# Optimization experiments

Hardware: AMD Instinct MI355X
Metric: run time of the kernel (lower is better)

Reference implementation:

```python
import jax, jax.numpy as jnp
import numpy as np

B, S, DMODEL, HEADS = 2, 2048, 1024, 16
DK = DMODEL // HEADS
DV = DMODEL // HEADS


def setup_inputs() -> dict:
    key = jax.random.key(0)
    kx, kq, kk, kv = jax.random.split(key, 4)
    x = jax.random.normal(kx, (B, S, DMODEL), dtype=jnp.float32)
    # stacked per-head projection weights, shape [H, dmodel, dk/dv]
    # (equivalent to nn.Linear(dmodel, dk, bias=False) per head)
    scale = 1.0 / np.sqrt(DMODEL)
    Wq = jax.random.uniform(kq, (HEADS, DMODEL, DK), jnp.float32, -scale, scale)
    Wk = jax.random.uniform(kk, (HEADS, DMODEL, DK), jnp.float32, -scale, scale)
    Wv = jax.random.uniform(kv, (HEADS, DMODEL, DV), jnp.float32, -scale, scale)
    return {"x": x, "Wq": Wq, "Wk": Wk, "Wv": Wv}


def reference(x, Wq, Wk, Wv):
    # per-head projections, batched across heads: [B,H,S,dk]
    q = jnp.einsum("bsd,hdk->bhsk", x, Wq)
    k = jnp.einsum("bsd,hdk->bhsk", x, Wk)
    v = jnp.einsum("bsd,hdv->bhsv", x, Wv)
    # NOTE: original module applies NO 1/sqrt(dk) scaling — keep faithful
    scores = jnp.einsum("bhqk,bhsk->bhqs", q, k)  # [B,H,S,S]
    attn = jax.nn.softmax(scores, axis=-1)
    out = jnp.einsum("bhqs,bhsv->bhqv", attn, v)  # [B,H,S,dv]
    # concat heads along last dim in head order
    Bsz, H, Sq, Dv = out.shape
    return jnp.transpose(out, (0, 2, 1, 3)).reshape(Bsz, Sq, H * Dv)
```

## Files before the change

### kernel.cpp

```cpp
#include <hip/hip_runtime.h>

#define B_ 2
#define S_ 2048
#define D_ 1024
#define H_ 16
#define DK_ 64
#define M_ (B_ * S_)
#define N_ (3 * D_)

typedef __bf16 bf16x8 __attribute__((ext_vector_type(8)));
typedef short s8vec __attribute__((ext_vector_type(8)));
typedef float f4vec __attribute__((ext_vector_type(4)));

static __device__ __forceinline__ ushort f2b(float f) {
  union { float f; unsigned u; } v; v.f = f;
  unsigned u = v.u;
  u += 0x7FFFu + ((u >> 16) & 1u);
  return (ushort)(u >> 16);
}

static __device__ __forceinline__ unsigned pk2(float a, float b) {
#if __has_builtin(__builtin_amdgcn_cvt_pk_bf16_f32)
  typedef __bf16 b2 __attribute__((ext_vector_type(2)));
  b2 r = __builtin_amdgcn_cvt_pk_bf16_f32(a, b);
  return __builtin_bit_cast(unsigned, r);
#else
  return (unsigned)f2b(a) | ((unsigned)f2b(b) << 16);
#endif
}

static __device__ __forceinline__ float fexp2(float x) {
#if __has_builtin(__builtin_amdgcn_exp2f)
  return __builtin_amdgcn_exp2f(x);
#else
  return exp2f(x);
#endif
}

static __device__ __forceinline__ f4vec mfma16(s8vec a, s8vec b, f4vec c) {
  return __builtin_amdgcn_mfma_f32_16x16x32_bf16(
      __builtin_bit_cast(bf16x8, a), __builtin_bit_cast(bf16x8, b), c, 0, 0, 0);
}

static __device__ __forceinline__ void gl_lds16(const ushort* g, ushort* l) {
  __builtin_amdgcn_global_load_lds(
      (const __attribute__((address_space(1))) unsigned*)g,
      (__attribute__((address_space(3))) unsigned*)l, 16, 0, 0);
}

static __device__ __forceinline__ void wg_barrier_lds() {
  asm volatile("" ::: "memory");
  __builtin_amdgcn_s_waitcnt(0xC07F);
  __builtin_amdgcn_s_barrier();
  asm volatile("" ::: "memory");
}

__global__ __launch_bounds__(256) void cvt_all(const float* __restrict__ x,
                                               const float* __restrict__ Wq,
                                               const float* __restrict__ Wk,
                                               const float* __restrict__ Wv,
                                               ushort* __restrict__ xb,
                                               ushort* __restrict__ wbt) {
  const int t = threadIdx.x;
  if (blockIdx.x < 4096) {
    int i = blockIdx.x * 256 + t;
    float4 v = ((const float4*)x)[i];
    ushort4 o;
    o.x = f2b(v.x); o.y = f2b(v.y); o.z = f2b(v.z); o.w = f2b(v.w);
    ((ushort4*)xb)[i] = o;
  } else {
    __shared__ ushort T[64 * 72];
    int bid = blockIdx.x - 4096;
    int w = bid >> 8, rem = bid & 255;
    int h = rem >> 4, d0 = (rem & 15) * 64;
    const float* W = (w == 0) ? Wq : (w == 1) ? Wk : Wv;
    const float* src = W + (size_t)h * 65536 + (size_t)d0 * 64;
#pragma unroll
    for (int j = 0; j < 4; ++j) {
      int idx = j * 256 + t;
      int dr = idx >> 4, kc = (idx & 15) * 4;
      float4 v = *(const float4*)(src + dr * 64 + kc);
      T[(kc + 0) * 72 + dr] = f2b(v.x);
      T[(kc + 1) * 72 + dr] = f2b(v.y);
      T[(kc + 2) * 72 + dr] = f2b(v.z);
      T[(kc + 3) * 72 + dr] = f2b(v.w);
    }
    __syncthreads();
    const int kk = t >> 2, dcg = (t & 3) * 16;
    ushort* dst = wbt + ((size_t)w * 1024 + h * 64 + kk) * 1024 + d0 + dcg;
    *(s8vec*)dst       = *(const s8vec*)&T[kk * 72 + dcg];
    *(s8vec*)(dst + 8) = *(const s8vec*)&T[kk * 72 + dcg + 8];
  }
}

__global__ __launch_bounds__(256) void proj_gemm(const ushort* __restrict__ xb,
                                                 const ushort* __restrict__ wbt,
                                                 ushort* __restrict__ qkv) {
  __shared__ __attribute__((aligned(16))) ushort As[128 * 64];
  __shared__ __attribute__((aligned(16))) ushort Bs[128 * 64];
  const int tid = threadIdx.x, wid = tid >> 6, lane = tid & 63;
  const int quad = lane >> 4, l15 = lane & 15;
  const int wm = wid & 1, wn = wid >> 1;
  const int m0 = blockIdx.x * 128, n0 = blockIdx.y * 128;

  f4vec acc[4][4];
#pragma unroll
  for (int mb = 0; mb < 4; mb++)
#pragma unroll
    for (int nb = 0; nb < 4; nb++)
#pragma unroll
      for (int i = 0; i < 4; i++) acc[mb][nb][i] = 0.f;

  const int sr = tid >> 3, sg = tid & 7;
  const int lg = sg ^ (sr & 7);
  const ushort* Ab = xb + (size_t)m0 * D_;
  const ushort* Bb = wbt + (size_t)n0 * D_;

  for (int k0 = 0; k0 < D_; k0 += 64) {
    __syncthreads();
#pragma unroll
    for (int j = 0; j < 4; ++j) {
      int r = j * 32 + sr;
      gl_lds16(Ab + (size_t)r * D_ + k0 + lg * 8, &As[j * 2048 + wid * 512]);
      gl_lds16(Bb + (size_t)r * D_ + k0 + lg * 8, &Bs[j * 2048 + wid * 512]);
    }
    __syncthreads();

#pragma unroll
    for (int kb = 0; kb < 2; ++kb) {
      s8vec af[4], bf[4];
#pragma unroll
      for (int mb = 0; mb < 4; ++mb) {
        int m = wm * 64 + mb * 16 + l15;
        int gpos = (kb * 4 + quad) ^ (m & 7);
        af[mb] = *(const s8vec*)&As[m * 64 + gpos * 8];
      }
#pragma unroll
      for (int nb = 0; nb < 4; ++nb) {
        int n = wn * 64 + nb * 16 + l15;
        int gpos = (kb * 4 + quad) ^ (n & 7);
        bf[nb] = *(const s8vec*)&Bs[n * 64 + gpos * 8];
      }
#pragma unroll
      for (int mb = 0; mb < 4; ++mb)
#pragma unroll
        for (int nb = 0; nb < 4; ++nb)
          acc[mb][nb] = mfma16(af[mb], bf[nb], acc[mb][nb]);
    }
  }

  const size_t per = (size_t)B_ * H_ * S_ * DK_;
  const int w = n0 >> 10;
  if (w == 2) {
    ushort* vt = qkv + 2 * per;
#pragma unroll
    for (int mb = 0; mb < 4; ++mb)
#pragma unroll
      for (int nb = 0; nb < 4; ++nb)
#pragma unroll
        for (int i = 0; i < 4; ++i) {
          int m = m0 + wm * 64 + mb * 16 + quad * 4 + i;
          int b = m >> 11, s = m & 2047;
          int n1 = (n0 & 1023) + wn * 64 + nb * 16 + l15;
          vt[((size_t)b * 1024 + n1) * S_ + s] = f2b(acc[mb][nb][i]);
        }
  } else {
    const float qs = (w == 0) ? 1.44269504f : 1.0f;
#pragma unroll
    for (int mb = 0; mb < 4; ++mb)
#pragma unroll
      for (int nb = 0; nb < 4; ++nb)
#pragma unroll
        for (int i = 0; i < 4; ++i) {
          int m = m0 + wm * 64 + mb * 16 + quad * 4 + i;
          int b = m >> 11, s = m & 2047;
          int n1 = (n0 & 1023) + wn * 64 + nb * 16 + l15;
          qkv[(size_t)w * per + (((size_t)b * H_ + (n1 >> 6)) * S_ + s) * 64 + (n1 & 63)] =
              f2b(acc[mb][nb][i] * qs);
        }
  }
}

__global__ __launch_bounds__(256) void attn(const ushort* __restrict__ qg,
                                            const ushort* __restrict__ kg,
                                            const ushort* __restrict__ vtg,
                                            float* __restrict__ out) {
  __shared__ __attribute__((aligned(16))) ushort Ks[64 * 64];
  __shared__ __attribute__((aligned(16))) ushort Vt[64 * 64];
  __shared__ __attribute__((aligned(16))) ushort Ps[4][32 * 128];
  const int qt = blockIdx.x, bh = blockIdx.y;
  const int b = bh >> 4, h = bh & 15;
  const int tid = threadIdx.x, wid = tid >> 6, lane = tid & 63;
  const int quad = lane >> 4, l15 = lane & 15, l7 = l15 & 7;

  const ushort* qbase = qg + ((size_t)bh * S_ + qt * 128 + wid * 32) * DK_;
  s8vec aq[2][2];
#pragma unroll
  for (int mb = 0; mb < 2; mb++) {
    aq[mb][0] = *(const s8vec*)(qbase + (size_t)(mb * 16 + l15) * DK_ + quad * 8);
    aq[mb][1] = *(const s8vec*)(qbase + (size_t)(mb * 16 + l15) * DK_ + 32 + quad * 8);
  }

  f4vec o[2][4];
  float lsum[2];
#pragma unroll
  for (int mb = 0; mb < 2; mb++) {
    lsum[mb] = 0.f;
#pragma unroll
    for (int nb = 0; nb < 4; nb++)
#pragma unroll
      for (int i = 0; i < 4; i++) o[mb][nb][i] = 0.f;
  }

  const int r = tid >> 3, gs = tid & 7;
  const int gk = gs ^ (r & 7);
  const ushort* kb_ = kg + (size_t)bh * S_ * DK_;
  const ushort* vb_ = vtg + (size_t)bh * 64 * S_;

  s8vec kpre[2], vpre[2];
  kpre[0] = *(const s8vec*)(kb_ + (size_t)r * DK_ + gk * 8);
  kpre[1] = *(const s8vec*)(kb_ + (size_t)(r + 32) * DK_ + gk * 8);
  vpre[0] = *(const s8vec*)(vb_ + (size_t)r * S_ + gk * 8);
  vpre[1] = *(const s8vec*)(vb_ + (size_t)(r + 32) * S_ + gk * 8);

  for (int kt = 0; kt < S_ / 64; ++kt) {
    wg_barrier_lds();
    *(s8vec*)&Ks[r * 64 + gs * 8]        = kpre[0];
    *(s8vec*)&Ks[(r + 32) * 64 + gs * 8] = kpre[1];
    *(s8vec*)&Vt[r * 64 + gs * 8]        = vpre[0];
    *(s8vec*)&Vt[(r + 32) * 64 + gs * 8] = vpre[1];
    if (kt + 1 < S_ / 64) {
      const ushort* kn = kb_ + (size_t)((kt + 1) * 64 + r) * DK_ + gk * 8;
      kpre[0] = *(const s8vec*)(kn);
      kpre[1] = *(const s8vec*)(kn + (size_t)32 * DK_);
      const ushort* vn = vb_ + (size_t)r * S_ + (kt + 1) * 64 + gk * 8;
      vpre[0] = *(const s8vec*)(vn);
      vpre[1] = *(const s8vec*)(vn + (size_t)32 * S_);
    }
    wg_barrier_lds();

    f4vec sct[2][4];
#pragma unroll
    for (int nb = 0; nb < 4; nb++) {
      const int row = nb * 16 + l15;
      s8vec ak0 = *(const s8vec*)&Ks[row * 64 + ((0 + quad) ^ l7) * 8];
      s8vec ak1 = *(const s8vec*)&Ks[row * 64 + ((4 + quad) ^ l7) * 8];
#pragma unroll
      for (int mb = 0; mb < 2; mb++) {
        f4vec z;
#pragma unroll
        for (int i = 0; i < 4; i++) z[i] = 0.f;
        z = mfma16(ak0, aq[mb][0], z);
        sct[mb][nb] = mfma16(ak1, aq[mb][1], z);
      }
    }

#pragma unroll
    for (int mb = 0; mb < 2; mb++) {
      const int q = mb * 16 + l15;
#pragma unroll
      for (int nb = 0; nb < 4; nb++) {
#pragma unroll
        for (int i = 0; i < 4; i++) {
          float p = fexp2(sct[mb][nb][i]);
          sct[mb][nb][i] = p;
          lsum[mb] += p;
        }
        unsigned p01 = pk2(sct[mb][nb][0], sct[mb][nb][1]);
        unsigned p23 = pk2(sct[mb][nb][2], sct[mb][nb][3]);
        const int c = (nb * 2 + (quad >> 1)) ^ l7;
        *(uint2*)&Ps[wid][q * 128 + c * 8 + (quad & 1) * 4] = make_uint2(p01, p23);
      }
    }

#pragma unroll
    for (int kc = 0; kc < 2; kc++) {
      s8vec ap[2];
#pragma unroll
      for (int mb = 0; mb < 2; mb++)
        ap[mb] = *(const s8vec*)&Ps[wid][(mb * 16 + l15) * 128 + (((kc * 4 + quad)) ^ l7) * 8];
#pragma unroll
      for (int nb = 0; nb < 4; nb++) {
        s8vec av = *(const s8vec*)&Vt[(nb * 16 + l15) * 64 + ((kc * 4 + quad) ^ l7) * 8];
        o[0][nb] = mfma16(av, ap[0], o[0][nb]);
        o[1][nb] = mfma16(av, ap[1], o[1][nb]);
      }
    }
  }

#pragma unroll
  for (int mb = 0; mb < 2; mb++) {
    lsum[mb] += __shfl_xor(lsum[mb], 16, 64);
    lsum[mb] += __shfl_xor(lsum[mb], 32, 64);
  }

#pragma unroll
  for (int mb = 0; mb < 2; mb++) {
    const float inv = 1.0f / lsum[mb];
    float* ob = out + ((size_t)b * S_ + qt * 128 + wid * 32 + mb * 16 + l15) * D_ + h * DK_;
#pragma unroll
    for (int nb = 0; nb < 4; nb++) {
      float4 v;
      v.x = o[mb][nb][0] * inv;
      v.y = o[mb][nb][1] * inv;
      v.z = o[mb][nb][2] * inv;
      v.w = o[mb][nb][3] * inv;
      *(float4*)(ob + nb * 16 + quad * 4) = v;
    }
  }
}

extern "C" void kernel_launch(void* const* d_in, const int* in_sizes, int n_in,
                              void* d_out, int out_size, void* d_ws, size_t ws_size,
                              hipStream_t stream) {
  const float* x  = (const float*)d_in[0];
  const float* Wq = (const float*)d_in[1];
  const float* Wk = (const float*)d_in[2];
  const float* Wv = (const float*)d_in[3];
  float* out = (float*)d_out;

  ushort* xb  = (ushort*)d_ws;
  ushort* wbt = xb + (size_t)B_ * S_ * D_;
  ushort* qkv = wbt + (size_t)3 * D_ * D_;
  const size_t per = (size_t)B_ * H_ * S_ * DK_;

  cvt_all<<<4096 + 768, 256, 0, stream>>>(x, Wq, Wk, Wv, xb, wbt);
  proj_gemm<<<dim3(M_ / 128, N_ / 128), 256, 0, stream>>>(xb, wbt, qkv);
  attn<<<dim3(S_ / 128, B_ * H_), 256, 0, stream>>>(qkv, qkv + per, qkv + 2 * per, out);
}
```

Measured before the change: 177.5 us.

## Split attention key range across two blocks and reduce partials

Adds a split-K dimension to the attention grid so each block handles half the key sequence, which doubles the block count from 512 to 1024 to fill the GPU better. Each half writes unnormalized fp32 partial outputs and row sums, and a new reduce kernel combines them. The row sum is now computed on the MFMA units by appending rows of ones to the V tile (an extra nb block) instead of scalar adds. The cost is extra global traffic for the fp32 partials and one more kernel launch. The workspace is reordered so the partials reuse the xb/wbt buffers.

```diff
diff --git a/kernel.cpp b/kernel.cpp
--- a/kernel.cpp
+++ b/kernel.cpp
@@ -184,14 +184,22 @@
 __global__ __launch_bounds__(256) void attn(const ushort* __restrict__ qg,
                                             const ushort* __restrict__ kg,
                                             const ushort* __restrict__ vtg,
-                                            float* __restrict__ out) {
+                                            float* __restrict__ opart,
+                                            float* __restrict__ lpart) {
   __shared__ __attribute__((aligned(16))) ushort Ks[64 * 64];
-  __shared__ __attribute__((aligned(16))) ushort Vt[64 * 64];
-  __shared__ __attribute__((aligned(16))) ushort Ps[4][32 * 128];
-  const int qt = blockIdx.x, bh = blockIdx.y;
+  __shared__ __attribute__((aligned(16))) ushort Vt[80 * 64];
+  __shared__ __attribute__((aligned(16))) ushort Ps[4][32 * 64];
+  const int qt = blockIdx.x, bh = blockIdx.y, ks = blockIdx.z;
   const int b = bh >> 4, h = bh & 15;
   const int tid = threadIdx.x, wid = tid >> 6, lane = tid & 63;
   const int quad = lane >> 4, l15 = lane & 15, l7 = l15 & 7;
+  const int kt0 = ks * (S_ / 128);
+
+  if (tid < 128) {
+    ushort* p = &Vt[(64 + (tid >> 3)) * 64 + (tid & 7) * 8];
+#pragma unroll
+    for (int j = 0; j < 8; ++j) p[j] = 0x3F80;
+  }
 
   const ushort* qbase = qg + ((size_t)bh * S_ + qt * 128 + wid * 32) * DK_;
   s8vec aq[2][2];
@@ -201,16 +209,13 @@
     aq[mb][1] = *(const s8vec*)(qbase + (size_t)(mb * 16 + l15) * DK_ + 32 + quad * 8);
   }
 
-  f4vec o[2][4];
-  float lsum[2];
-#pragma unroll
-  for (int mb = 0; mb < 2; mb++) {
-    lsum[mb] = 0.f;
-#pragma unroll
-    for (int nb = 0; nb < 4; nb++)
+  f4vec o[2][5];
+#pragma unroll
+  for (int mb = 0; mb < 2; mb++)
+#pragma unroll
+    for (int nb = 0; nb < 5; nb++)
 #pragma unroll
       for (int i = 0; i < 4; i++) o[mb][nb][i] = 0.f;
-  }
 
   const int r = tid >> 3, gs = tid & 7;
   const int gk = gs ^ (r & 7);
@@ -218,18 +223,18 @@
   const ushort* vb_ = vtg + (size_t)bh * 64 * S_;
 
   s8vec kpre[2], vpre[2];
-  kpre[0] = *(const s8vec*)(kb_ + (size_t)r * DK_ + gk * 8);
-  kpre[1] = *(const s8vec*)(kb_ + (size_t)(r + 32) * DK_ + gk * 8);
-  vpre[0] = *(const s8vec*)(vb_ + (size_t)r * S_ + gk * 8);
-  vpre[1] = *(const s8vec*)(vb_ + (size_t)(r + 32) * S_ + gk * 8);
-
-  for (int kt = 0; kt < S_ / 64; ++kt) {
+  kpre[0] = *(const s8vec*)(kb_ + (size_t)(kt0 * 64 + r) * DK_ + gk * 8);
+  kpre[1] = *(const s8vec*)(kb_ + (size_t)(kt0 * 64 + r + 32) * DK_ + gk * 8);
+  vpre[0] = *(const s8vec*)(vb_ + (size_t)r * S_ + kt0 * 64 + gk * 8);
+  vpre[1] = *(const s8vec*)(vb_ + (size_t)(r + 32) * S_ + kt0 * 64 + gk * 8);
+
+  for (int kt = kt0; kt < kt0 + S_ / 128; ++kt) {
     wg_barrier_lds();
     *(s8vec*)&Ks[r * 64 + gs * 8]        = kpre[0];
     *(s8vec*)&Ks[(r + 32) * 64 + gs * 8] = kpre[1];
     *(s8vec*)&Vt[r * 64 + gs * 8]        = vpre[0];
     *(s8vec*)&Vt[(r + 32) * 64 + gs * 8] = vpre[1];
-    if (kt + 1 < S_ / 64) {
+    if (kt + 1 < kt0 + S_ / 128) {
       const ushort* kn = kb_ + (size_t)((kt + 1) * 64 + r) * DK_ + gk * 8;
       kpre[0] = *(const s8vec*)(kn);
       kpre[1] = *(const s8vec*)(kn + (size_t)32 * DK_);
@@ -260,16 +265,13 @@
       const int q = mb * 16 + l15;
 #pragma unroll
       for (int nb = 0; nb < 4; nb++) {
-#pragma unroll
-        for (int i = 0; i < 4; i++) {
-          float p = fexp2(sct[mb][nb][i]);
-          sct[mb][nb][i] = p;
-          lsum[mb] += p;
-        }
-        unsigned p01 = pk2(sct[mb][nb][0], sct[mb][nb][1]);
-        unsigned p23 = pk2(sct[mb][nb][2], sct[mb][nb][3]);
+        f4vec p;
+#pragma unroll
+        for (int i = 0; i < 4; i++) p[i] = fexp2(sct[mb][nb][i]);
+        unsigned p01 = pk2(p[0], p[1]);
+        unsigned p23 = pk2(p[2], p[3]);
         const int c = (nb * 2 + (quad >> 1)) ^ l7;
-        *(uint2*)&Ps[wid][q * 128 + c * 8 + (quad & 1) * 4] = make_uint2(p01, p23);
+        *(uint2*)&Ps[wid][q * 64 + c * 8 + (quad & 1) * 4] = make_uint2(p01, p23);
       }
     }
 
@@ -278,9 +280,9 @@
       s8vec ap[2];
 #pragma unroll
       for (int mb = 0; mb < 2; mb++)
-        ap[mb] = *(const s8vec*)&Ps[wid][(mb * 16 + l15) * 128 + (((kc * 4 + quad)) ^ l7) * 8];
-#pragma unroll
-      for (int nb = 0; nb < 4; nb++) {
+        ap[mb] = *(const s8vec*)&Ps[wid][(mb * 16 + l15) * 64 + ((kc * 4 + quad) ^ l7) * 8];
+#pragma unroll
+      for (int nb = 0; nb < 5; nb++) {
         s8vec av = *(const s8vec*)&Vt[(nb * 16 + l15) * 64 + ((kc * 4 + quad) ^ l7) * 8];
         o[0][nb] = mfma16(av, ap[0], o[0][nb]);
         o[1][nb] = mfma16(av, ap[1], o[1][nb]);
@@ -288,26 +290,40 @@
     }
   }
 
+  float* ob = opart + (size_t)ks * (M_ * (size_t)D_);
 #pragma unroll
   for (int mb = 0; mb < 2; mb++) {
-    lsum[mb] += __shfl_xor(lsum[mb], 16, 64);
-    lsum[mb] += __shfl_xor(lsum[mb], 32, 64);
-  }
-
-#pragma unroll
-  for (int mb = 0; mb < 2; mb++) {
-    const float inv = 1.0f / lsum[mb];
-    float* ob = out + ((size_t)b * S_ + qt * 128 + wid * 32 + mb * 16 + l15) * D_ + h * DK_;
+    const int s = qt * 128 + wid * 32 + mb * 16 + l15;
+    float* orow = ob + ((size_t)b * S_ + s) * D_ + h * DK_;
 #pragma unroll
     for (int nb = 0; nb < 4; nb++) {
       float4 v;
-      v.x = o[mb][nb][0] * inv;
-      v.y = o[mb][nb][1] * inv;
-      v.z = o[mb][nb][2] * inv;
-      v.w = o[mb][nb][3] * inv;
-      *(float4*)(ob + nb * 16 + quad * 4) = v;
-    }
-  }
+      v.x = o[mb][nb][0]; v.y = o[mb][nb][1];
+      v.z = o[mb][nb][2]; v.w = o[mb][nb][3];
+      *(float4*)(orow + nb * 16 + quad * 4) = v;
+    }
+    if (quad == 0)
+      lpart[(size_t)ks * 65536 + (size_t)bh * S_ + s] = o[mb][4][0];
+  }
+}
+
+__global__ __launch_bounds__(256) void attn_reduce(const float* __restrict__ opart,
+                                                   const float* __restrict__ lpart,
+                                                   float* __restrict__ out) {
+  const int i = blockIdx.x * 256 + threadIdx.x;
+  const float4 a = ((const float4*)opart)[i];
+  const float4 c = ((const float4*)(opart + (size_t)M_ * D_))[i];
+  const int e = i * 4;
+  const int row = e >> 10;
+  const int d = e & 1023;
+  const int idx = ((row >> 11) * 16 + (d >> 6)) * S_ + (row & 2047);
+  const float inv = 1.0f / (lpart[idx] + lpart[65536 + idx]);
+  float4 rv;
+  rv.x = (a.x + c.x) * inv;
+  rv.y = (a.y + c.y) * inv;
+  rv.z = (a.z + c.z) * inv;
+  rv.w = (a.w + c.w) * inv;
+  ((float4*)out)[i] = rv;
 }
 
 extern "C" void kernel_launch(void* const* d_in, const int* in_sizes, int n_in,
@@ -319,12 +335,16 @@
   const float* Wv = (const float*)d_in[3];
   float* out = (float*)d_out;
 
-  ushort* xb  = (ushort*)d_ws;
+  ushort* qkv = (ushort*)d_ws;
+  const size_t per = (size_t)B_ * H_ * S_ * DK_;
+  ushort* xb  = qkv + 3 * per;
   ushort* wbt = xb + (size_t)B_ * S_ * D_;
-  ushort* qkv = wbt + (size_t)3 * D_ * D_;
-  const size_t per = (size_t)B_ * H_ * S_ * DK_;
+  float* opart = (float*)xb;
+  float* lpart = opart + (size_t)2 * M_ * D_;
 
   cvt_all<<<4096 + 768, 256, 0, stream>>>(x, Wq, Wk, Wv, xb, wbt);
   proj_gemm<<<dim3(M_ / 128, N_ / 128), 256, 0, stream>>>(xb, wbt, qkv);
-  attn<<<dim3(S_ / 128, B_ * H_), 256, 0, stream>>>(qkv, qkv + per, qkv + 2 * per, out);
-}
+  attn<<<dim3(S_ / 128, B_ * H_, 2), 256, 0, stream>>>(qkv, qkv + per, qkv + 2 * per,
+                                                       opart, lpart);
+  attn_reduce<<<(M_ * D_) / 4 / 256, 256, 0, stream>>>(opart, lpart, out);
+}
```

Result: slower. 184.0 us (+3.7%).
